# Kernel optimization log

Measured on AMD Instinct MI355X. Metric: run time of the kernel, lower is better.

The kernel has to match this reference:

```python
import jax, jax.numpy as jnp
import numpy as np

N = 50000
IN_DIM = 256
HID = 64
HEADS = 4
OUT_DIM = 64
E = 800000
SLOPE = 0.2


def gat_conv(x, src, dst, W, a_src, a_dst, bias, heads, out_ch):
    """PyG-style GATConv: gather -> edge attention -> segment softmax -> scatter.
    x: [N, in], W: [in, heads*out_ch], a_src/a_dst: [heads, out_ch], bias: [heads*out_ch].
    Returns [N, heads*out_ch] (heads concatenated)."""
    n = x.shape[0]
    h = (x @ W).reshape(n, heads, out_ch)               # [N, H, C]
    s = jnp.einsum('nhc,hc->nh', h, a_src)              # [N, H]
    d = jnp.einsum('nhc,hc->nh', h, a_dst)              # [N, H]
    e = jax.nn.leaky_relu(s[src] + d[dst], SLOPE)       # [E, H]
    emax = jax.ops.segment_max(e, dst, num_segments=n)  # stable softmax per dst
    ex = jnp.exp(e - emax[dst])
    denom = jax.ops.segment_sum(ex, dst, num_segments=n)
    alpha = ex / (denom[dst] + 1e-16)                   # [E, H]
    msg = h[src] * alpha[:, :, None]                    # [E, H, C]
    out = jax.ops.segment_sum(msg, dst, num_segments=n) # [N, H, C]
    return out.reshape(n, heads * out_ch) + bias


def setup_inputs() -> dict:
    key = jax.random.key(0)
    ks = jax.random.split(key, 12)
    x = jax.random.normal(ks[0], (N, IN_DIM), dtype=jnp.float32)
    edge_index = jax.random.randint(ks[1], (2, E), 0, N, dtype=jnp.int64)
    sc = 0.1
    params = {
        'W1': jax.random.normal(ks[2], (IN_DIM, HEADS * HID), dtype=jnp.float32) * sc,
        'a_src1': jax.random.normal(ks[3], (HEADS, HID), dtype=jnp.float32) * sc,
        'a_dst1': jax.random.normal(ks[4], (HEADS, HID), dtype=jnp.float32) * sc,
        'b1': jnp.zeros((HEADS * HID,), dtype=jnp.float32),
        'W2': jax.random.normal(ks[5], (HEADS * HID, HID), dtype=jnp.float32) * sc,
        'a_src2': jax.random.normal(ks[6], (1, HID), dtype=jnp.float32) * sc,
        'a_dst2': jax.random.normal(ks[7], (1, HID), dtype=jnp.float32) * sc,
        'b2': jnp.zeros((HID,), dtype=jnp.float32),
        'Wf1': jax.random.normal(ks[8], (HID, HID), dtype=jnp.float32) * sc,
        'bf1': jnp.zeros((HID,), dtype=jnp.float32),
        'Wf2': jax.random.normal(ks[9], (HID, OUT_DIM), dtype=jnp.float32) * sc,
        'bf2': jnp.zeros((OUT_DIM,), dtype=jnp.float32),
    }
    return {'x': x, 'edge_index': edge_index, **params}


def reference(x, edge_index, W1, a_src1, a_dst1, b1, W2, a_src2, a_dst2, b2,
              Wf1, bf1, Wf2, bf2):
    n = x.shape[0]
    # PyG GATConv adds self-loops by default
    loops = jnp.arange(n, dtype=edge_index.dtype)
    src = jnp.concatenate([edge_index[0], loops])
    dst = jnp.concatenate([edge_index[1], loops])
    h = jax.nn.relu(gat_conv(x, src, dst, W1, a_src1, a_dst1, b1, HEADS, HID))
    h = jax.nn.relu(gat_conv(h, src, dst, W2, a_src2, a_dst2, b2, 1, HID))
    h = jax.nn.relu(h @ Wf1 + bf1)
    return jax.nn.softmax(h @ Wf2 + bf2, axis=1)
```

## Files before the change

kernel.cpp:

```cpp
#include <hip/hip_runtime.h>

#define NNODES 50000
#define NEDGES 800000
#define INDIM  256
#define HIDC   64
#define HEADS  4
static constexpr int ETOT = NEDGES + NNODES;

typedef _Float16 half4 __attribute__((ext_vector_type(4)));
typedef _Float16 half8 __attribute__((ext_vector_type(8)));
typedef short    s16x8 __attribute__((ext_vector_type(8)));
typedef short    s16x4 __attribute__((ext_vector_type(4)));
typedef float    f32x4 __attribute__((ext_vector_type(4)));

__device__ __forceinline__ unsigned short f2bf(float f) {
    unsigned u = __float_as_uint(f);
    u += 0x7fffu + ((u >> 16) & 1u);
    return (unsigned short)(u >> 16);
}
__device__ __forceinline__ float bf2f(unsigned short h) {
    return __uint_as_float(((unsigned)h) << 16);
}

__global__ void detect_k(const unsigned* __restrict__ ei32, int* __restrict__ flag) {
    __shared__ int any32;
    if (threadIdx.x == 0) any32 = 0;
    __syncthreads();
    if (ei32[1 + 2 * threadIdx.x] != 0u) any32 = 1;
    __syncthreads();
    if (threadIdx.x == 0) *flag = !any32;
}

__device__ __forceinline__ int load_idx(const void* ei, int is64, size_t pos) {
    return is64 ? (int)((const long long*)ei)[pos] : ((const int*)ei)[pos];
}

__global__ __launch_bounds__(256)
void hist_k(const void* __restrict__ ei, const int* __restrict__ flag,
            int* __restrict__ count) {
    int e = blockIdx.x * 256 + threadIdx.x;
    if (e >= ETOT) return;
    int is64 = *flag;
    int dst = (e < NEDGES) ? load_idx(ei, is64, (size_t)NEDGES + e) : (e - NEDGES);
    atomicAdd(&count[dst], 1);
}

__global__ __launch_bounds__(1024)
void scan1_k(const int* __restrict__ count, int* __restrict__ rowptr,
             int* __restrict__ bsum, int n) {
    __shared__ int wsum[16];
    const int tid = threadIdx.x;
    const int lane = tid & 63;
    const int w = tid >> 6;
    int i = blockIdx.x * 1024 + tid;
    int v = (i < n) ? count[i] : 0;
    int x = v;
    #pragma unroll
    for (int dd = 1; dd < 64; dd <<= 1) {
        int y = __shfl_up(x, dd);
        if (lane >= dd) x += y;
    }
    if (lane == 63) wsum[w] = x;
    __syncthreads();
    int woff = 0, total = 0;
    #pragma unroll
    for (int j = 0; j < 16; ++j) {
        if (j < w) woff += wsum[j];
        total += wsum[j];
    }
    if (i < n) rowptr[i] = woff + x - v;
    if (tid == 0) bsum[blockIdx.x] = total;
}

__global__ void scan2_k(int* __restrict__ bsum, int* __restrict__ bpre, int nb,
                        int* __restrict__ rowptr, int n) {
    int lane = threadIdx.x;
    int v = (lane < nb) ? bsum[lane] : 0;
    int x = v;
    #pragma unroll
    for (int dd = 1; dd < 64; dd <<= 1) {
        int y = __shfl_up(x, dd);
        if (lane >= dd) x += y;
    }
    if (lane < nb) bpre[lane] = x - v;
    if (lane == 63) rowptr[n] = x;
}

__global__ __launch_bounds__(1024)
void scan3_k(int* __restrict__ rowptr, const int* __restrict__ bpre, int n) {
    int i = blockIdx.x * 1024 + threadIdx.x;
    if (i < n) rowptr[i] += bpre[blockIdx.x];
}

__global__ __launch_bounds__(256)
void scatter_k(const void* __restrict__ ei, const int* __restrict__ flag,
               const int* __restrict__ rowptr, int* __restrict__ fill,
               int* __restrict__ csr_src) {
    int e = blockIdx.x * 256 + threadIdx.x;
    if (e >= ETOT) return;
    int is64 = *flag;
    int src, dst;
    if (e < NEDGES) {
        src = load_idx(ei, is64, (size_t)e);
        dst = load_idx(ei, is64, (size_t)NEDGES + e);
    } else {
        src = e - NEDGES; dst = src;
    }
    int pos = rowptr[dst] + atomicAdd(&fill[dst], 1);
    csr_src[pos] = src;
}

__global__ __launch_bounds__(256)
void convw_k(const float* __restrict__ W, unsigned short* __restrict__ t_hi,
             unsigned short* __restrict__ t_lo, int K, int N) {
    int idx = blockIdx.x * 256 + threadIdx.x;
    if (idx >= K * N) return;
    int k = idx / N, n = idx % N;
    float w = W[idx];
    unsigned short hi = f2bf(w);
    unsigned short lo = f2bf(w - bf2f(hi));
    t_hi[(size_t)n * K + k] = hi;
    t_lo[(size_t)n * K + k] = lo;
}

template<int BN, int SD>
__global__ __launch_bounds__(256)
void gemm_mfma_k(const float* __restrict__ A,
                 const unsigned short* __restrict__ Bt_hi,
                 const unsigned short* __restrict__ Bt_lo,
                 float* __restrict__ C, _Float16* __restrict__ Ch,
                 const float* __restrict__ asrc, const float* __restrict__ adst,
                 float* __restrict__ S, float* __restrict__ D,
                 int M, int N, int K) {
    constexpr int CB = BN / 32;
    constexpr int BI = (BN * 4) / 256;
    __shared__ unsigned short sAh[128][40], sAl[128][40];
    __shared__ unsigned short sBh[BN][40], sBl[BN][40];
    const int tid = threadIdx.x;
    const int bm = blockIdx.y * 128;
    const int bn = blockIdx.x * BN;
    const int w = tid >> 6, lane = tid & 63;
    const int wr = w >> 1, wc = w & 1;
    const int lr = lane & 15, lk = lane >> 4;

    f32x4 acc[4][CB] = {};

    for (int k0 = 0; k0 < K; k0 += 32) {
        float4 av[4];
        #pragma unroll
        for (int i = 0; i < 4; ++i) {
            int idx = tid + 256 * i;
            int row = idx >> 3, c4 = idx & 7;
            int grow = bm + row; if (grow >= M) grow = M - 1;
            av[i] = *(const float4*)(A + (size_t)grow * K + k0 + c4 * 4);
        }
        s16x8 bhv[BI], blv[BI];
        #pragma unroll
        for (int i = 0; i < BI; ++i) {
            int idx = tid + 256 * i;
            int col = idx >> 2, ch = idx & 3;
            bhv[i] = *(const s16x8*)(Bt_hi + (size_t)(bn + col) * K + k0 + ch * 8);
            blv[i] = *(const s16x8*)(Bt_lo + (size_t)(bn + col) * K + k0 + ch * 8);
        }
        __syncthreads();
        #pragma unroll
        for (int i = 0; i < 4; ++i) {
            int idx = tid + 256 * i;
            int row = idx >> 3, c4 = idx & 7;
            float vs[4] = {av[i].x, av[i].y, av[i].z, av[i].w};
            unsigned short h[4], l[4];
            #pragma unroll
            for (int j = 0; j < 4; ++j) {
                h[j] = f2bf(vs[j]);
                l[j] = f2bf(vs[j] - bf2f(h[j]));
            }
            *(s16x4*)&sAh[row][c4 * 4] = (s16x4){(short)h[0], (short)h[1], (short)h[2], (short)h[3]};
            *(s16x4*)&sAl[row][c4 * 4] = (s16x4){(short)l[0], (short)l[1], (short)l[2], (short)l[3]};
        }
        #pragma unroll
        for (int i = 0; i < BI; ++i) {
            int idx = tid + 256 * i;
            int col = idx >> 2, ch = idx & 3;
            *(s16x8*)&sBh[col][ch * 8] = bhv[i];
            *(s16x8*)&sBl[col][ch * 8] = blv[i];
        }
        __syncthreads();
        s16x8 afh[4], afl[4], bfh[CB], bfl[CB];
        #pragma unroll
        for (int rb = 0; rb < 4; ++rb) {
            int row = wr * 64 + rb * 16 + lr;
            afh[rb] = *(const s16x8*)&sAh[row][lk * 8];
            afl[rb] = *(const s16x8*)&sAl[row][lk * 8];
        }
        #pragma unroll
        for (int cb = 0; cb < CB; ++cb) {
            int col = wc * (BN / 2) + cb * 16 + lr;
            bfh[cb] = *(const s16x8*)&sBh[col][lk * 8];
            bfl[cb] = *(const s16x8*)&sBl[col][lk * 8];
        }
        #pragma unroll
        for (int rb = 0; rb < 4; ++rb)
            #pragma unroll
            for (int cb = 0; cb < CB; ++cb) {
                acc[rb][cb] = __builtin_amdgcn_mfma_f32_16x16x32_bf16(afh[rb], bfh[cb], acc[rb][cb], 0, 0, 0);
                acc[rb][cb] = __builtin_amdgcn_mfma_f32_16x16x32_bf16(afh[rb], bfl[cb], acc[rb][cb], 0, 0, 0);
                acc[rb][cb] = __builtin_amdgcn_mfma_f32_16x16x32_bf16(afl[rb], bfh[cb], acc[rb][cb], 0, 0, 0);
            }
    }
    #pragma unroll
    for (int rb = 0; rb < 4; ++rb)
        #pragma unroll
        for (int cb = 0; cb < CB; ++cb)
            #pragma unroll
            for (int r = 0; r < 4; ++r) {
                int row = bm + wr * 64 + rb * 16 + lk * 4 + r;
                int col = bn + wc * (BN / 2) + cb * 16 + lr;
                if (row < M) {
                    float v = acc[rb][cb][r];
                    if constexpr (SD == 0) C[(size_t)row * N + col] = v;
                    if (Ch) Ch[(size_t)row * N + col] = (_Float16)v;
                }
            }
    if constexpr (SD != 0) {
        float af[CB], df[CB];
        #pragma unroll
        for (int cb = 0; cb < CB; ++cb) {
            int colg = bn + wc * (BN / 2) + cb * 16 + lr;
            af[cb] = asrc[colg];
            df[cb] = adst[colg];
        }
        #pragma unroll
        for (int rb = 0; rb < 4; ++rb)
            #pragma unroll
            for (int r = 0; r < 4; ++r) {
                float ps = 0.f, pd = 0.f;
                #pragma unroll
                for (int cb = 0; cb < CB; ++cb) {
                    ps += acc[rb][cb][r] * af[cb];
                    pd += acc[rb][cb][r] * df[cb];
                }
                #pragma unroll
                for (int m = 1; m < 16; m <<= 1) {
                    ps += __shfl_xor(ps, m);
                    pd += __shfl_xor(pd, m);
                }
                int row = bm + wr * 64 + rb * 16 + lk * 4 + r;
                if (lr == 0 && row < M) {
                    if constexpr (SD == 1) {
                        int head = (bn + wc * (BN / 2)) >> 6;
                        S[(size_t)row * (N >> 6) + head] = ps;
                        D[(size_t)row * (N >> 6) + head] = pd;
                    } else {
                        atomicAdd(&S[row], ps);
                        atomicAdd(&D[row], pd);
                    }
                }
            }
    }
}

template<int H>
__global__ __launch_bounds__(256)
void sd_k(const float* __restrict__ hfeat, const float* __restrict__ a_src,
          const float* __restrict__ a_dst, float* __restrict__ s,
          float* __restrict__ d, int n) {
    const int lane = threadIdx.x & 63;
    const int node = blockIdx.x * 4 + (threadIdx.x >> 6);
    if (node >= n) return;
    const float* row = hfeat + (size_t)node * (H * 64);
    #pragma unroll
    for (int h = 0; h < H; ++h) {
        float f = row[h * 64 + lane];
        float vs = f * a_src[h * 64 + lane];
        float vd = f * a_dst[h * 64 + lane];
        #pragma unroll
        for (int m = 32; m; m >>= 1) {
            vs += __shfl_xor(vs, m);
            vd += __shfl_xor(vd, m);
        }
        if (lane == 0) { s[node * H + h] = vs; d[node * H + h] = vd; }
    }
}

__device__ __forceinline__ float leaky(float e) { return (e > 0.f) ? e : 0.2f * e; }

__device__ __forceinline__ float sel4(const float v[4], int idx) {
    float r = v[0];
    r = (idx == 1) ? v[1] : r;
    r = (idx == 2) ? v[2] : r;
    r = (idx == 3) ? v[3] : r;
    return r;
}

__device__ __forceinline__ void osm_upd(float& m, float& sm, float e) {
    float nm = fmaxf(m, e);
    sm = sm * __expf(m - nm) + __expf(e - nm);
    m = nm;
}

template<int H, bool EB>
__global__ __launch_bounds__(256)
void agg_k(const float* __restrict__ hfeat, const _Float16* __restrict__ hhalf,
           const float* __restrict__ s, const float* __restrict__ d,
           const float* __restrict__ bias, const int* __restrict__ rowptr,
           const int* __restrict__ csr_src, float* __restrict__ ebuf,
           float* __restrict__ out, int n) {
    const int lane = threadIdx.x & 63;
    const int node = blockIdx.x * 4 + (threadIdx.x >> 6);
    if (node >= n) return;
    const int beg = rowptr[node];
    const int end = rowptr[node + 1];
    float dh[H], dn[H], inv[H];
    #pragma unroll
    for (int h = 0; h < H; ++h) {
        dh[h] = d[node * H + h];
        dn[h] = 0.f;
    }

    if constexpr (EB) {
        for (int i = beg + lane; i < end; i += 64) {
            int sidx = csr_src[i];
            if constexpr (H == 4) {
                float4 sv = *(const float4*)(s + (size_t)sidx * 4);
                float4 ex;
                ex.x = __expf(leaky(sv.x + dh[0]));
                ex.y = __expf(leaky(sv.y + dh[1]));
                ex.z = __expf(leaky(sv.z + dh[2]));
                ex.w = __expf(leaky(sv.w + dh[3]));
                *(float4*)(ebuf + (size_t)i * 4) = ex;
                dn[0] += ex.x; dn[1] += ex.y; dn[2] += ex.z; dn[3] += ex.w;
            } else {
                float ex = __expf(leaky(s[sidx] + dh[0]));
                ebuf[i] = ex;
                dn[0] += ex;
            }
        }
        #pragma unroll
        for (int h = 0; h < H; ++h) {
            #pragma unroll
            for (int m = 32; m; m >>= 1) dn[h] += __shfl_xor(dn[h], m);
            inv[h] = 1.f / (dn[h] + 1e-16f);
        }

        if constexpr (H == 4) {
            const half8* H8 = (const half8*)hhalf;
            const int sub = lane >> 5;
            const int c8 = lane & 31;
            const int head = c8 >> 3;
            const float invh = sel4(inv, head);
            float acc[8] = {};
            int i = beg;
            for (; i + 7 < end; i += 8) {
                int e0 = i + sub, e1 = i + 2 + sub, e2 = i + 4 + sub, e3 = i + 6 + sub;
                int s0 = csr_src[e0], s1 = csr_src[e1];
                int s2 = csr_src[e2], s3 = csr_src[e3];
                float x0 = ebuf[(size_t)e0 * 4 + head];
                float x1 = ebuf[(size_t)e1 * 4 + head];
                float x2 = ebuf[(size_t)e2 * 4 + head];
                float x3 = ebuf[(size_t)e3 * 4 + head];
                half8 h0 = H8[(size_t)s0 * 32 + c8];
                half8 h1 = H8[(size_t)s1 * 32 + c8];
                half8 h2 = H8[(size_t)s2 * 32 + c8];
                half8 h3 = H8[(size_t)s3 * 32 + c8];
                #pragma unroll
                for (int j = 0; j < 8; ++j)
                    acc[j] += x0 * (float)h0[j] + x1 * (float)h1[j]
                            + x2 * (float)h2[j] + x3 * (float)h3[j];
            }
            for (; i < end; i += 2) {
                int e = i + sub;
                if (e < end) {
                    int s0 = csr_src[e];
                    float x = ebuf[(size_t)e * 4 + head];
                    half8 hh = H8[(size_t)s0 * 32 + c8];
                    #pragma unroll
                    for (int j = 0; j < 8; ++j) acc[j] += x * (float)hh[j];
                }
            }
            #pragma unroll
            for (int j = 0; j < 8; ++j) acc[j] += __shfl_xor(acc[j], 32);
            if (lane < 32) {
                float4 b0 = *(const float4*)(bias + c8 * 8);
                float4 b1 = *(const float4*)(bias + c8 * 8 + 4);
                float4 o0, o1;
                o0.x = fmaxf(acc[0] * invh + b0.x, 0.f);
                o0.y = fmaxf(acc[1] * invh + b0.y, 0.f);
                o0.z = fmaxf(acc[2] * invh + b0.z, 0.f);
                o0.w = fmaxf(acc[3] * invh + b0.w, 0.f);
                o1.x = fmaxf(acc[4] * invh + b1.x, 0.f);
                o1.y = fmaxf(acc[5] * invh + b1.y, 0.f);
                o1.z = fmaxf(acc[6] * invh + b1.z, 0.f);
                o1.w = fmaxf(acc[7] * invh + b1.w, 0.f);
                *(float4*)(out + (size_t)node * 256 + c8 * 8) = o0;
                *(float4*)(out + (size_t)node * 256 + c8 * 8 + 4) = o1;
            }
        } else {
            const half8* H8 = (const half8*)hhalf;
            const int sub = lane >> 3;
            const int c8 = lane & 7;
            float acc[8] = {};
            int i = beg;
            for (; i + 15 < end; i += 16) {
                int e0 = i + sub, e1 = i + 8 + sub;
                int s0 = csr_src[e0], s1 = csr_src[e1];
                float x0 = ebuf[e0], x1 = ebuf[e1];
                half8 h0 = H8[(size_t)s0 * 8 + c8];
                half8 h1 = H8[(size_t)s1 * 8 + c8];
                #pragma unroll
                for (int j = 0; j < 8; ++j)
                    acc[j] += x0 * (float)h0[j] + x1 * (float)h1[j];
            }
            for (; i < end; i += 8) {
                int e = i + sub;
                if (e < end) {
                    int s0 = csr_src[e];
                    float x = ebuf[e];
                    half8 hh = H8[(size_t)s0 * 8 + c8];
                    #pragma unroll
                    for (int j = 0; j < 8; ++j) acc[j] += x * (float)hh[j];
                }
            }
            #pragma unroll
            for (int m = 8; m <= 32; m <<= 1)
                #pragma unroll
                for (int j = 0; j < 8; ++j) acc[j] += __shfl_xor(acc[j], m);
            if (lane < 8) {
                float4 b0 = *(const float4*)(bias + c8 * 8);
                float4 b1 = *(const float4*)(bias + c8 * 8 + 4);
                float4 o0, o1;
                o0.x = fmaxf(acc[0] * inv[0] + b0.x, 0.f);
                o0.y = fmaxf(acc[1] * inv[0] + b0.y, 0.f);
                o0.z = fmaxf(acc[2] * inv[0] + b0.z, 0.f);
                o0.w = fmaxf(acc[3] * inv[0] + b0.w, 0.f);
                o1.x = fmaxf(acc[4] * inv[0] + b1.x, 0.f);
                o1.y = fmaxf(acc[5] * inv[0] + b1.y, 0.f);
                o1.z = fmaxf(acc[6] * inv[0] + b1.z, 0.f);
                o1.w = fmaxf(acc[7] * inv[0] + b1.w, 0.f);
                *(float4*)(out + (size_t)node * 64 + c8 * 8) = o0;
                *(float4*)(out + (size_t)node * 64 + c8 * 8 + 4) = o1;
            }
        }
    } else {
        float mx[H], sm[H];
        #pragma unroll
        for (int h = 0; h < H; ++h) { mx[h] = -3.0e38f; sm[h] = 0.f; }
        for (int i = beg + lane; i < end; i += 64) {
            int sidx = csr_src[i];
            if constexpr (H == 4) {
                float4 sv = *(const float4*)(s + (size_t)sidx * 4);
                osm_upd(mx[0], sm[0], leaky(sv.x + dh[0]));
                osm_upd(mx[1], sm[1], leaky(sv.y + dh[1]));
                osm_upd(mx[2], sm[2], leaky(sv.z + dh[2]));
                osm_upd(mx[3], sm[3], leaky(sv.w + dh[3]));
            } else {
                osm_upd(mx[0], sm[0], leaky(s[sidx] + dh[0]));
            }
        }
        #pragma unroll
        for (int h = 0; h < H; ++h) {
            #pragma unroll
            for (int dd = 32; dd; dd >>= 1) {
                float om = __shfl_xor(mx[h], dd);
                float os = __shfl_xor(sm[h], dd);
                float nm = fmaxf(mx[h], om);
                sm[h] = sm[h] * __expf(mx[h] - nm) + os * __expf(om - nm);
                mx[h] = nm;
            }
            inv[h] = 1.f / (sm[h] + 1e-16f);
        }
        if constexpr (H == 4) {
            const int head = lane >> 4;
            const float invh = sel4(inv, head);
            const float mxh = sel4(mx, head);
            const float dhh = sel4(dh, head);
            const float4* H4 = (const float4*)hfeat;
            float4 acc = {0.f, 0.f, 0.f, 0.f};
            for (int i = beg; i < end; ++i) {
                int s0 = csr_src[i];
                float al0 = __expf(leaky(s[(size_t)s0 * 4 + head] + dhh) - mxh) * invh;
                float4 h0 = H4[(size_t)s0 * 64 + lane];
                acc.x += al0 * h0.x; acc.y += al0 * h0.y;
                acc.z += al0 * h0.z; acc.w += al0 * h0.w;
            }
            float4 bv = ((const float4*)bias)[lane];
            float4 o;
            o.x = fmaxf(acc.x + bv.x, 0.f); o.y = fmaxf(acc.y + bv.y, 0.f);
            o.z = fmaxf(acc.z + bv.z, 0.f); o.w = fmaxf(acc.w + bv.w, 0.f);
            ((float4*)out)[(size_t)node * 64 + lane] = o;
        } else {
            float acc = 0.f;
            for (int i = beg; i < end; ++i) {
                int s0 = csr_src[i];
                float a0 = __expf(leaky(s[s0] + dh[0]) - mx[0]) * inv[0];
                acc += a0 * hfeat[(size_t)s0 * 64 + lane];
            }
            float v = acc + bias[lane];
            out[(size_t)node * 64 + lane] = fmaxf(v, 0.f);
        }
    }
}

__global__ __launch_bounds__(256)
void ffm_k(const float* __restrict__ in,
           const unsigned short* __restrict__ w1h, const unsigned short* __restrict__ w1l,
           const float* __restrict__ bf1,
           const unsigned short* __restrict__ w2h, const unsigned short* __restrict__ w2l,
           const float* __restrict__ bf2, float* __restrict__ out, int M) {
    __shared__ unsigned short sAh[64][80], sAl[64][80];
    __shared__ unsigned short sW1h[64][80], sW1l[64][80];
    __shared__ unsigned short sW2h[64][80], sW2l[64][80];
    const int tid = threadIdx.x;
    const int bm = blockIdx.x * 64;
    const int w = tid >> 6, lane = tid & 63;
    const int lr = lane & 15, lk = lane >> 4;

    for (int c = tid; c < 512; c += 256) {
        int n = c >> 3, k8 = c & 7;
        int dcol = (k8 >> 2) * 40 + (k8 & 3) * 8;
        *(s16x8*)&sW1h[n][dcol] = *(const s16x8*)(w1h + n * 64 + k8 * 8);
        *(s16x8*)&sW1l[n][dcol] = *(const s16x8*)(w1l + n * 64 + k8 * 8);
        *(s16x8*)&sW2h[n][dcol] = *(const s16x8*)(w2h + n * 64 + k8 * 8);
        *(s16x8*)&sW2l[n][dcol] = *(const s16x8*)(w2l + n * 64 + k8 * 8);
    }
    #pragma unroll
    for (int i = 0; i < 4; ++i) {
        int c = tid + 256 * i;
        int row = c >> 4, c4 = c & 15;
        int grow = bm + row; if (grow >= M) grow = M - 1;
        float4 av = *(const float4*)(in + (size_t)grow * 64 + c4 * 4);
        float vs[4] = {av.x, av.y, av.z, av.w};
        unsigned short h[4], l[4];
        #pragma unroll
        for (int j = 0; j < 4; ++j) {
            h[j] = f2bf(vs[j]);
            l[j] = f2bf(vs[j] - bf2f(h[j]));
        }
        int dcol = (c4 >> 3) * 40 + (c4 & 7) * 4;
        *(s16x4*)&sAh[row][dcol] = (s16x4){(short)h[0], (short)h[1], (short)h[2], (short)h[3]};
        *(s16x4*)&sAl[row][dcol] = (s16x4){(short)l[0], (short)l[1], (short)l[2], (short)l[3]};
    }
    __syncthreads();
    f32x4 a1[4] = {};
    #pragma unroll
    for (int ks = 0; ks < 2; ++ks) {
        int koff = ks * 40 + lk * 8;
        s16x8 ah = *(const s16x8*)&sAh[w * 16 + lr][koff];
        s16x8 al = *(const s16x8*)&sAl[w * 16 + lr][koff];
        #pragma unroll
        for (int cb = 0; cb < 4; ++cb) {
            s16x8 bh = *(const s16x8*)&sW1h[cb * 16 + lr][koff];
            s16x8 bl = *(const s16x8*)&sW1l[cb * 16 + lr][koff];
            a1[cb] = __builtin_amdgcn_mfma_f32_16x16x32_bf16(ah, bh, a1[cb], 0, 0, 0);
            a1[cb] = __builtin_amdgcn_mfma_f32_16x16x32_bf16(ah, bl, a1[cb], 0, 0, 0);
            a1[cb] = __builtin_amdgcn_mfma_f32_16x16x32_bf16(al, bh, a1[cb], 0, 0, 0);
        }
    }
    __syncthreads();
    #pragma unroll
    for (int cb = 0; cb < 4; ++cb) {
        int col = cb * 16 + lr;
        float b = bf1[col];
        int dcol = (col >> 5) * 40 + (col & 31);
        #pragma unroll
        for (int r = 0; r < 4; ++r) {
            int row = w * 16 + lk * 4 + r;
            float y = fmaxf(a1[cb][r] + b, 0.f);
            unsigned short hh = f2bf(y);
            sAh[row][dcol] = hh;
            sAl[row][dcol] = f2bf(y - bf2f(hh));
        }
    }
    __syncthreads();
    f32x4 a2[4] = {};
    #pragma unroll
    for (int ks = 0; ks < 2; ++ks) {
        int koff = ks * 40 + lk * 8;
        s16x8 ah = *(const s16x8*)&sAh[w * 16 + lr][koff];
        s16x8 al = *(const s16x8*)&sAl[w * 16 + lr][koff];
        #pragma unroll
        for (int cb = 0; cb < 4; ++cb) {
            s16x8 bh = *(const s16x8*)&sW2h[cb * 16 + lr][koff];
            s16x8 bl = *(const s16x8*)&sW2l[cb * 16 + lr][koff];
            a2[cb] = __builtin_amdgcn_mfma_f32_16x16x32_bf16(ah, bh, a2[cb], 0, 0, 0);
            a2[cb] = __builtin_amdgcn_mfma_f32_16x16x32_bf16(ah, bl, a2[cb], 0, 0, 0);
            a2[cb] = __builtin_amdgcn_mfma_f32_16x16x32_bf16(al, bh, a2[cb], 0, 0, 0);
        }
    }
    float zb[4];
    #pragma unroll
    for (int cb = 0; cb < 4; ++cb) zb[cb] = bf2[cb * 16 + lr];
    #pragma unroll
    for (int r = 0; r < 4; ++r) {
        int row = bm + w * 16 + lk * 4 + r;
        float z0 = a2[0][r] + zb[0], z1 = a2[1][r] + zb[1];
        float z2 = a2[2][r] + zb[2], z3 = a2[3][r] + zb[3];
        float m = fmaxf(fmaxf(z0, z1), fmaxf(z2, z3));
        #pragma unroll
        for (int dd = 1; dd < 16; dd <<= 1) m = fmaxf(m, __shfl_xor(m, dd));
        float e0 = __expf(z0 - m), e1 = __expf(z1 - m);
        float e2 = __expf(z2 - m), e3 = __expf(z3 - m);
        float sum = e0 + e1 + e2 + e3;
        #pragma unroll
        for (int dd = 1; dd < 16; dd <<= 1) sum += __shfl_xor(sum, dd);
        float is = 1.f / sum;
        if (row < M) {
            out[(size_t)row * 64 + 0 + lr]  = e0 * is;
            out[(size_t)row * 64 + 16 + lr] = e1 * is;
            out[(size_t)row * 64 + 32 + lr] = e2 * is;
            out[(size_t)row * 64 + 48 + lr] = e3 * is;
        }
    }
}

__global__ __launch_bounds__(256)
void ff_k(const float* __restrict__ in, const float* __restrict__ Wf1,
          const float* __restrict__ bf1, const float* __restrict__ Wf2,
          const float* __restrict__ bf2, float* __restrict__ out, int n) {
    __shared__ float w1[64 * 64];
    __shared__ float w2[64 * 64];
    __shared__ float xrow[4][64];
    __shared__ float yrow[4][64];
    const int tid = threadIdx.x;
    for (int i = tid; i < 64 * 64; i += 256) { w1[i] = Wf1[i]; w2[i] = Wf2[i]; }
    __syncthreads();
    const int wv = tid >> 6;
    const int lane = tid & 63;
    const float B1 = bf1[lane], B2 = bf2[lane];
    const int nblk = (n + 3) / 4;
    for (int nb = blockIdx.x; nb < nblk; nb += gridDim.x) {
        int node = nb * 4 + wv;
        int nd = node < n ? node : (n - 1);
        float x = in[(size_t)nd * 64 + lane];
        xrow[wv][lane] = x;
        float y = B1;
        #pragma unroll 8
        for (int k = 0; k < 64; ++k) y += xrow[wv][k] * w1[k * 64 + lane];
        y = fmaxf(y, 0.f);
        yrow[wv][lane] = y;
        float z = B2;
        #pragma unroll 8
        for (int k = 0; k < 64; ++k) z += yrow[wv][k] * w2[k * 64 + lane];
        float m = z;
        #pragma unroll
        for (int dd = 32; dd; dd >>= 1) m = fmaxf(m, __shfl_xor(m, dd));
        float ex = __expf(z - m);
        float sum = ex;
        #pragma unroll
        for (int dd = 32; dd; dd >>= 1) sum += __shfl_xor(sum, dd);
        if (node < n) out[(size_t)node * 64 + lane] = ex / sum;
    }
}

extern "C" void kernel_launch(void* const* d_in, const int* in_sizes, int n_in,
                              void* d_out, int out_size, void* d_ws, size_t ws_size,
                              hipStream_t stream) {
    const float* x      = (const float*)d_in[0];
    const void*  ei     = d_in[1];
    const float* W1     = (const float*)d_in[2];
    const float* a_src1 = (const float*)d_in[3];
    const float* a_dst1 = (const float*)d_in[4];
    const float* b1     = (const float*)d_in[5];
    const float* W2     = (const float*)d_in[6];
    const float* a_src2 = (const float*)d_in[7];
    const float* a_dst2 = (const float*)d_in[8];
    const float* b2     = (const float*)d_in[9];
    const float* Wf1    = (const float*)d_in[10];
    const float* bf1    = (const float*)d_in[11];
    const float* Wf2    = (const float*)d_in[12];
    const float* bf2    = (const float*)d_in[13];
    float* outp = (float*)d_out;

    char* ws = (char*)d_ws;
    size_t off = 0;
    auto take = [&](size_t bytes) -> char* {
        char* p = ws + off;
        off += (bytes + 255) & ~(size_t)255;
        return p;
    };
    int*   flag   = (int*)take(4);
    int*   count  = (int*)take((size_t)NNODES * 4);
    int*   fill   = (int*)take((size_t)NNODES * 4);
    int*   rowptr = (int*)take((size_t)(NNODES + 1) * 4);
    int*   bsum   = (int*)take(64 * 4);
    int*   bpre   = (int*)take(64 * 4);
    int*   csr    = (int*)take((size_t)ETOT * 4);
    unsigned short* w1t_hi = (unsigned short*)take((size_t)256 * 256 * 2);
    unsigned short* w1t_lo = (unsigned short*)take((size_t)256 * 256 * 2);
    unsigned short* w2t_hi = (unsigned short*)take((size_t)64 * 256 * 2);
    unsigned short* w2t_lo = (unsigned short*)take((size_t)64 * 256 * 2);
    unsigned short* wf1t_hi = (unsigned short*)take((size_t)64 * 64 * 2);
    unsigned short* wf1t_lo = (unsigned short*)take((size_t)64 * 64 * 2);
    unsigned short* wf2t_hi = (unsigned short*)take((size_t)64 * 64 * 2);
    unsigned short* wf2t_lo = (unsigned short*)take((size_t)64 * 64 * 2);
    float* h1     = (float*)take((size_t)NNODES * 256 * 4);
    float* agg1   = (float*)take((size_t)NNODES * 256 * 4);
    float* s1     = (float*)take((size_t)NNODES * HEADS * 4);
    float* d1     = (float*)take((size_t)NNODES * HEADS * 4);
    float* ebuf   = (float*)take((size_t)ETOT * HEADS * 4);
    _Float16* h1h = (_Float16*)take((size_t)NNODES * 256 * 2);
    const bool eb_ok = (off <= ws_size);
    float*    h2   = h1;
    float*    s2   = s1;
    float*    d2   = d1;
    float*    agg2 = agg1;
    _Float16* h2h  = h1h;

    detect_k<<<1, 128, 0, stream>>>((const unsigned*)ei, flag);
    hipMemsetAsync(count, 0, (size_t)NNODES * 4, stream);
    hipMemsetAsync(fill, 0, (size_t)NNODES * 4, stream);
    const int eblocks = (ETOT + 255) / 256;
    hist_k<<<eblocks, 256, 0, stream>>>(ei, flag, count);
    const int sblocks = (NNODES + 1023) / 1024;
    scan1_k<<<sblocks, 1024, 0, stream>>>(count, rowptr, bsum, NNODES);
    scan2_k<<<1, 64, 0, stream>>>(bsum, bpre, sblocks, rowptr, NNODES);
    scan3_k<<<sblocks, 1024, 0, stream>>>(rowptr, bpre, NNODES);
    scatter_k<<<eblocks, 256, 0, stream>>>(ei, flag, rowptr, fill, csr);

    convw_k<<<(256 * 256) / 256, 256, 0, stream>>>(W1, w1t_hi, w1t_lo, 256, 256);
    convw_k<<<(256 * 64) / 256, 256, 0, stream>>>(W2, w2t_hi, w2t_lo, 256, 64);
    convw_k<<<(64 * 64) / 256, 256, 0, stream>>>(Wf1, wf1t_hi, wf1t_lo, 64, 64);
    convw_k<<<(64 * 64) / 256, 256, 0, stream>>>(Wf2, wf2t_hi, wf2t_lo, 64, 64);

    const int nodeblocks = NNODES / 4;
    const int mblocks = (NNODES + 127) / 128;
    const dim3 gg1(2, mblocks);
    const dim3 gg2(1, mblocks);

    if (eb_ok) {
        gemm_mfma_k<128, 1><<<gg1, 256, 0, stream>>>(x, w1t_hi, w1t_lo,
            nullptr, h1h, a_src1, a_dst1, s1, d1, NNODES, 256, 256);
        agg_k<HEADS, true><<<nodeblocks, 256, 0, stream>>>(h1, h1h, s1, d1, b1,
            rowptr, csr, ebuf, agg1, NNODES);

        hipMemsetAsync(s2, 0, (size_t)NNODES * 4, stream);
        hipMemsetAsync(d2, 0, (size_t)NNODES * 4, stream);
        gemm_mfma_k<64, 2><<<gg2, 256, 0, stream>>>(agg1, w2t_hi, w2t_lo,
            nullptr, h2h, a_src2, a_dst2, s2, d2, NNODES, 64, 256);
        agg_k<1, true><<<nodeblocks, 256, 0, stream>>>(h2, h2h, s2, d2, b2,
            rowptr, csr, ebuf, agg2, NNODES);

        ffm_k<<<(NNODES + 63) / 64, 256, 0, stream>>>(agg2, wf1t_hi, wf1t_lo,
            bf1, wf2t_hi, wf2t_lo, bf2, outp, NNODES);
    } else {
        gemm_mfma_k<128, 0><<<gg1, 256, 0, stream>>>(x, w1t_hi, w1t_lo,
            h1, nullptr, nullptr, nullptr, nullptr, nullptr, NNODES, 256, 256);
        sd_k<HEADS><<<nodeblocks, 256, 0, stream>>>(h1, a_src1, a_dst1, s1, d1, NNODES);
        agg_k<HEADS, false><<<nodeblocks, 256, 0, stream>>>(h1, h1h, s1, d1, b1,
            rowptr, csr, ebuf, agg1, NNODES);
        gemm_mfma_k<64, 0><<<gg2, 256, 0, stream>>>(agg1, w2t_hi, w2t_lo,
            h2, nullptr, nullptr, nullptr, nullptr, nullptr, NNODES, 64, 256);
        sd_k<1><<<nodeblocks, 256, 0, stream>>>(h2, a_src2, a_dst2, s2, d2, NNODES);
        agg_k<1, false><<<nodeblocks, 256, 0, stream>>>(h2, h2h, s2, d2, b2,
            rowptr, csr, ebuf, agg2, NNODES);
        ff_k<<<1024, 256, 0, stream>>>(agg2, Wf1, bf1, Wf2, bf2, outp, NNODES);
    }
}
```

Before: 291.7 us.

## Drop edge buffer, stage edge weights in LDS, merge setup launches

The aggregation kernel no longer writes per-edge exp values to a global edge buffer and rereads them. It now processes each node's edges in chunks of 64, keeping source indices and exp weights in per-wave shared memory, and normalises by the denominator only at the end. Several small launches are also merged: the index-width detection is inlined into the edge kernels, the four weight conversions become one kernel, and paired memsets are combined. The fallback path and the fp32 feature buffers are removed. Relying on s_waitcnt rather than a barrier for the wave-private LDS is a subtle correctness assumption.

```diff
diff --git a/kernel.cpp b/kernel.cpp
--- a/kernel.cpp
+++ b/kernel.cpp
@@ -7,7 +7,6 @@
 #define HEADS  4
 static constexpr int ETOT = NEDGES + NNODES;
 
-typedef _Float16 half4 __attribute__((ext_vector_type(4)));
 typedef _Float16 half8 __attribute__((ext_vector_type(8)));
 typedef short    s16x8 __attribute__((ext_vector_type(8)));
 typedef short    s16x4 __attribute__((ext_vector_type(4)));
@@ -22,13 +21,11 @@
     return __uint_as_float(((unsigned)h) << 16);
 }
 
-__global__ void detect_k(const unsigned* __restrict__ ei32, int* __restrict__ flag) {
-    __shared__ int any32;
-    if (threadIdx.x == 0) any32 = 0;
-    __syncthreads();
-    if (ei32[1 + 2 * threadIdx.x] != 0u) any32 = 1;
-    __syncthreads();
-    if (threadIdx.x == 0) *flag = !any32;
+__device__ __forceinline__ int is_int64(const unsigned* __restrict__ ei32) {
+    int r = 1;
+    #pragma unroll
+    for (int i = 1; i < 64; i += 2) r &= (ei32[i] == 0u);
+    return r;
 }
 
 __device__ __forceinline__ int load_idx(const void* ei, int is64, size_t pos) {
@@ -36,11 +33,10 @@
 }
 
 __global__ __launch_bounds__(256)
-void hist_k(const void* __restrict__ ei, const int* __restrict__ flag,
-            int* __restrict__ count) {
+void hist_k(const void* __restrict__ ei, int* __restrict__ count) {
     int e = blockIdx.x * 256 + threadIdx.x;
     if (e >= ETOT) return;
-    int is64 = *flag;
+    int is64 = is_int64((const unsigned*)ei);
     int dst = (e < NEDGES) ? load_idx(ei, is64, (size_t)NEDGES + e) : (e - NEDGES);
     atomicAdd(&count[dst], 1);
 }
@@ -93,12 +89,11 @@
 }
 
 __global__ __launch_bounds__(256)
-void scatter_k(const void* __restrict__ ei, const int* __restrict__ flag,
-               const int* __restrict__ rowptr, int* __restrict__ fill,
-               int* __restrict__ csr_src) {
+void scatter_k(const void* __restrict__ ei, const int* __restrict__ rowptr,
+               int* __restrict__ fill, int* __restrict__ csr_src) {
     int e = blockIdx.x * 256 + threadIdx.x;
     if (e >= ETOT) return;
-    int is64 = *flag;
+    int is64 = is_int64((const unsigned*)ei);
     int src, dst;
     if (e < NEDGES) {
         src = load_idx(ei, is64, (size_t)e);
@@ -111,16 +106,25 @@
 }
 
 __global__ __launch_bounds__(256)
-void convw_k(const float* __restrict__ W, unsigned short* __restrict__ t_hi,
-             unsigned short* __restrict__ t_lo, int K, int N) {
+void convall_k(const float* __restrict__ W1, const float* __restrict__ W2,
+               const float* __restrict__ Wf1, const float* __restrict__ Wf2,
+               unsigned short* __restrict__ w1h, unsigned short* __restrict__ w1l,
+               unsigned short* __restrict__ w2h, unsigned short* __restrict__ w2l,
+               unsigned short* __restrict__ f1h, unsigned short* __restrict__ f1l,
+               unsigned short* __restrict__ f2h, unsigned short* __restrict__ f2l) {
     int idx = blockIdx.x * 256 + threadIdx.x;
-    if (idx >= K * N) return;
+    const float* W; unsigned short *th, *tl; int K, N;
+    if (idx < 65536)       { W = W1;  th = w1h; tl = w1l; K = 256; N = 256; }
+    else if (idx < 81920)  { idx -= 65536; W = W2;  th = w2h; tl = w2l; K = 256; N = 64; }
+    else if (idx < 86016)  { idx -= 81920; W = Wf1; th = f1h; tl = f1l; K = 64;  N = 64; }
+    else if (idx < 90112)  { idx -= 86016; W = Wf2; th = f2h; tl = f2l; K = 64;  N = 64; }
+    else return;
     int k = idx / N, n = idx % N;
-    float w = W[idx];
+    float w = W[(size_t)k * N + n];
     unsigned short hi = f2bf(w);
     unsigned short lo = f2bf(w - bf2f(hi));
-    t_hi[(size_t)n * K + k] = hi;
-    t_lo[(size_t)n * K + k] = lo;
+    th[(size_t)n * K + k] = hi;
+    tl[(size_t)n * K + k] = lo;
 }
 
 template<int BN, int SD>
@@ -128,7 +132,7 @@
 void gemm_mfma_k(const float* __restrict__ A,
                  const unsigned short* __restrict__ Bt_hi,
                  const unsigned short* __restrict__ Bt_lo,
-                 float* __restrict__ C, _Float16* __restrict__ Ch,
+                 _Float16* __restrict__ Ch,
                  const float* __restrict__ asrc, const float* __restrict__ adst,
                  float* __restrict__ S, float* __restrict__ D,
                  int M, int N, int K) {
@@ -215,13 +219,9 @@
             for (int r = 0; r < 4; ++r) {
                 int row = bm + wr * 64 + rb * 16 + lk * 4 + r;
                 int col = bn + wc * (BN / 2) + cb * 16 + lr;
-                if (row < M) {
-                    float v = acc[rb][cb][r];
-                    if constexpr (SD == 0) C[(size_t)row * N + col] = v;
-                    if (Ch) Ch[(size_t)row * N + col] = (_Float16)v;
-                }
-            }
-    if constexpr (SD != 0) {
+                if (row < M) Ch[(size_t)row * N + col] = (_Float16)acc[rb][cb][r];
+            }
+    {
         float af[CB], df[CB];
         #pragma unroll
         for (int cb = 0; cb < CB; ++cb) {
@@ -259,29 +259,6 @@
     }
 }
 
-template<int H>
-__global__ __launch_bounds__(256)
-void sd_k(const float* __restrict__ hfeat, const float* __restrict__ a_src,
-          const float* __restrict__ a_dst, float* __restrict__ s,
-          float* __restrict__ d, int n) {
-    const int lane = threadIdx.x & 63;
-    const int node = blockIdx.x * 4 + (threadIdx.x >> 6);
-    if (node >= n) return;
-    const float* row = hfeat + (size_t)node * (H * 64);
-    #pragma unroll
-    for (int h = 0; h < H; ++h) {
-        float f = row[h * 64 + lane];
-        float vs = f * a_src[h * 64 + lane];
-        float vd = f * a_dst[h * 64 + lane];
-        #pragma unroll
-        for (int m = 32; m; m >>= 1) {
-            vs += __shfl_xor(vs, m);
-            vd += __shfl_xor(vd, m);
-        }
-        if (lane == 0) { s[node * H + h] = vs; d[node * H + h] = vd; }
-    }
-}
-
 __device__ __forceinline__ float leaky(float e) { return (e > 0.f) ? e : 0.2f * e; }
 
 __device__ __forceinline__ float sel4(const float v[4], int idx) {
@@ -292,210 +269,154 @@
     return r;
 }
 
-__device__ __forceinline__ void osm_upd(float& m, float& sm, float e) {
-    float nm = fmaxf(m, e);
-    sm = sm * __expf(m - nm) + __expf(e - nm);
-    m = nm;
-}
-
-template<int H, bool EB>
+template<int H>
 __global__ __launch_bounds__(256)
-void agg_k(const float* __restrict__ hfeat, const _Float16* __restrict__ hhalf,
+void agg_k(const _Float16* __restrict__ hhalf,
            const float* __restrict__ s, const float* __restrict__ d,
            const float* __restrict__ bias, const int* __restrict__ rowptr,
-           const int* __restrict__ csr_src, float* __restrict__ ebuf,
-           float* __restrict__ out, int n) {
+           const int* __restrict__ csr_src, float* __restrict__ out, int n) {
+    __shared__ float exs[4][H][64];
+    __shared__ int   srcs[4][64];
     const int lane = threadIdx.x & 63;
-    const int node = blockIdx.x * 4 + (threadIdx.x >> 6);
+    const int wv   = threadIdx.x >> 6;
+    const int node = blockIdx.x * 4 + wv;
     if (node >= n) return;
-    const int beg = rowptr[node];
-    const int end = rowptr[node + 1];
-    float dh[H], dn[H], inv[H];
-    #pragma unroll
-    for (int h = 0; h < H; ++h) {
-        dh[h] = d[node * H + h];
-        dn[h] = 0.f;
-    }
-
-    if constexpr (EB) {
-        for (int i = beg + lane; i < end; i += 64) {
-            int sidx = csr_src[i];
-            if constexpr (H == 4) {
+    const int beg = rowptr[node], end = rowptr[node + 1];
+    float dh[H], dn[H];
+    #pragma unroll
+    for (int h = 0; h < H; ++h) { dh[h] = d[node * H + h]; dn[h] = 0.f; }
+    const half8* H8 = (const half8*)hhalf;
+
+    if constexpr (H == 4) {
+        const int sub = lane >> 5, c8 = lane & 31, head = c8 >> 3;
+        float acc[8] = {};
+        for (int c0 = beg; c0 < end; c0 += 64) {
+            const int cend = (c0 + 64 < end) ? c0 + 64 : end;
+            int e = c0 + lane;
+            if (e < end) {
+                int sidx = csr_src[e];
                 float4 sv = *(const float4*)(s + (size_t)sidx * 4);
-                float4 ex;
-                ex.x = __expf(leaky(sv.x + dh[0]));
-                ex.y = __expf(leaky(sv.y + dh[1]));
-                ex.z = __expf(leaky(sv.z + dh[2]));
-                ex.w = __expf(leaky(sv.w + dh[3]));
-                *(float4*)(ebuf + (size_t)i * 4) = ex;
-                dn[0] += ex.x; dn[1] += ex.y; dn[2] += ex.z; dn[3] += ex.w;
-            } else {
-                float ex = __expf(leaky(s[sidx] + dh[0]));
-                ebuf[i] = ex;
-                dn[0] += ex;
-            }
-        }
-        #pragma unroll
-        for (int h = 0; h < H; ++h) {
-            #pragma unroll
-            for (int m = 32; m; m >>= 1) dn[h] += __shfl_xor(dn[h], m);
-            inv[h] = 1.f / (dn[h] + 1e-16f);
-        }
-
-        if constexpr (H == 4) {
-            const half8* H8 = (const half8*)hhalf;
-            const int sub = lane >> 5;
-            const int c8 = lane & 31;
-            const int head = c8 >> 3;
-            const float invh = sel4(inv, head);
-            float acc[8] = {};
-            int i = beg;
-            for (; i + 7 < end; i += 8) {
-                int e0 = i + sub, e1 = i + 2 + sub, e2 = i + 4 + sub, e3 = i + 6 + sub;
-                int s0 = csr_src[e0], s1 = csr_src[e1];
-                int s2 = csr_src[e2], s3 = csr_src[e3];
-                float x0 = ebuf[(size_t)e0 * 4 + head];
-                float x1 = ebuf[(size_t)e1 * 4 + head];
-                float x2 = ebuf[(size_t)e2 * 4 + head];
-                float x3 = ebuf[(size_t)e3 * 4 + head];
+                float e0 = __expf(leaky(sv.x + dh[0]));
+                float e1 = __expf(leaky(sv.y + dh[1]));
+                float e2 = __expf(leaky(sv.z + dh[2]));
+                float e3 = __expf(leaky(sv.w + dh[3]));
+                srcs[wv][lane] = sidx;
+                exs[wv][0][lane] = e0; exs[wv][1][lane] = e1;
+                exs[wv][2][lane] = e2; exs[wv][3][lane] = e3;
+                dn[0] += e0; dn[1] += e1; dn[2] += e2; dn[3] += e3;
+            }
+            asm volatile("s_waitcnt lgkmcnt(0)" ::: "memory");
+            int i = c0;
+            for (; i + 7 < cend; i += 8) {
+                int j = i - c0 + sub;
+                int s0 = srcs[wv][j],     s1 = srcs[wv][j + 2];
+                int s2 = srcs[wv][j + 4], s3 = srcs[wv][j + 6];
+                float x0 = exs[wv][head][j],     x1 = exs[wv][head][j + 2];
+                float x2 = exs[wv][head][j + 4], x3 = exs[wv][head][j + 6];
                 half8 h0 = H8[(size_t)s0 * 32 + c8];
                 half8 h1 = H8[(size_t)s1 * 32 + c8];
                 half8 h2 = H8[(size_t)s2 * 32 + c8];
                 half8 h3 = H8[(size_t)s3 * 32 + c8];
                 #pragma unroll
-                for (int j = 0; j < 8; ++j)
-                    acc[j] += x0 * (float)h0[j] + x1 * (float)h1[j]
-                            + x2 * (float)h2[j] + x3 * (float)h3[j];
-            }
-            for (; i < end; i += 2) {
-                int e = i + sub;
-                if (e < end) {
-                    int s0 = csr_src[e];
-                    float x = ebuf[(size_t)e * 4 + head];
+                for (int q = 0; q < 8; ++q)
+                    acc[q] += x0 * (float)h0[q] + x1 * (float)h1[q]
+                            + x2 * (float)h2[q] + x3 * (float)h3[q];
+            }
+            for (; i < cend; i += 2) {
+                int e2i = i + sub;
+                if (e2i < cend) {
+                    int j = e2i - c0;
+                    int s0 = srcs[wv][j];
+                    float x = exs[wv][head][j];
                     half8 hh = H8[(size_t)s0 * 32 + c8];
                     #pragma unroll
-                    for (int j = 0; j < 8; ++j) acc[j] += x * (float)hh[j];
+                    for (int q = 0; q < 8; ++q) acc[q] += x * (float)hh[q];
                 }
             }
+        }
+        float inv_[4];
+        #pragma unroll
+        for (int h = 0; h < 4; ++h) {
             #pragma unroll
-            for (int j = 0; j < 8; ++j) acc[j] += __shfl_xor(acc[j], 32);
-            if (lane < 32) {
-                float4 b0 = *(const float4*)(bias + c8 * 8);
-                float4 b1 = *(const float4*)(bias + c8 * 8 + 4);
-                float4 o0, o1;
-                o0.x = fmaxf(acc[0] * invh + b0.x, 0.f);
-                o0.y = fmaxf(acc[1] * invh + b0.y, 0.f);
-                o0.z = fmaxf(acc[2] * invh + b0.z, 0.f);
-                o0.w = fmaxf(acc[3] * invh + b0.w, 0.f);
-                o1.x = fmaxf(acc[4] * invh + b1.x, 0.f);
-                o1.y = fmaxf(acc[5] * invh + b1.y, 0.f);
-                o1.z = fmaxf(acc[6] * invh + b1.z, 0.f);
-                o1.w = fmaxf(acc[7] * invh + b1.w, 0.f);
-                *(float4*)(out + (size_t)node * 256 + c8 * 8) = o0;
-                *(float4*)(out + (size_t)node * 256 + c8 * 8 + 4) = o1;
-            }
-        } else {
-            const half8* H8 = (const half8*)hhalf;
-            const int sub = lane >> 3;
-            const int c8 = lane & 7;
-            float acc[8] = {};
-            int i = beg;
-            for (; i + 15 < end; i += 16) {
-                int e0 = i + sub, e1 = i + 8 + sub;
-                int s0 = csr_src[e0], s1 = csr_src[e1];
-                float x0 = ebuf[e0], x1 = ebuf[e1];
+            for (int m = 32; m; m >>= 1) dn[h] += __shfl_xor(dn[h], m);
+            inv_[h] = 1.f / (dn[h] + 1e-16f);
+        }
+        const float invh = sel4(inv_, head);
+        #pragma unroll
+        for (int q = 0; q < 8; ++q) acc[q] += __shfl_xor(acc[q], 32);
+        if (lane < 32) {
+            float4 b0 = *(const float4*)(bias + c8 * 8);
+            float4 b1 = *(const float4*)(bias + c8 * 8 + 4);
+            float4 o0, o1;
+            o0.x = fmaxf(acc[0] * invh + b0.x, 0.f);
+            o0.y = fmaxf(acc[1] * invh + b0.y, 0.f);
+            o0.z = fmaxf(acc[2] * invh + b0.z, 0.f);
+            o0.w = fmaxf(acc[3] * invh + b0.w, 0.f);
+            o1.x = fmaxf(acc[4] * invh + b1.x, 0.f);
+            o1.y = fmaxf(acc[5] * invh + b1.y, 0.f);
+            o1.z = fmaxf(acc[6] * invh + b1.z, 0.f);
+            o1.w = fmaxf(acc[7] * invh + b1.w, 0.f);
+            *(float4*)(out + (size_t)node * 256 + c8 * 8) = o0;
+            *(float4*)(out + (size_t)node * 256 + c8 * 8 + 4) = o1;
+        }
+    } else {
+        const int sub = lane >> 3, c8 = lane & 7;
+        float acc[8] = {};
+        for (int c0 = beg; c0 < end; c0 += 64) {
+            const int cend = (c0 + 64 < end) ? c0 + 64 : end;
+            int e = c0 + lane;
+            if (e < end) {
+                int sidx = csr_src[e];
+                float ex = __expf(leaky(s[sidx] + dh[0]));
+                srcs[wv][lane] = sidx;
+                exs[wv][0][lane] = ex;
+                dn[0] += ex;
+            }
+            asm volatile("s_waitcnt lgkmcnt(0)" ::: "memory");
+            int i = c0;
+            for (; i + 15 < cend; i += 16) {
+                int j = i - c0 + sub;
+                int s0 = srcs[wv][j], s1 = srcs[wv][j + 8];
+                float x0 = exs[wv][0][j], x1 = exs[wv][0][j + 8];
                 half8 h0 = H8[(size_t)s0 * 8 + c8];
                 half8 h1 = H8[(size_t)s1 * 8 + c8];
                 #pragma unroll
-                for (int j = 0; j < 8; ++j)
-                    acc[j] += x0 * (float)h0[j] + x1 * (float)h1[j];
-            }
-            for (; i < end; i += 8) {
-                int e = i + sub;
-                if (e < end) {
-                    int s0 = csr_src[e];
-                    float x = ebuf[e];
+                for (int q = 0; q < 8; ++q)
+                    acc[q] += x0 * (float)h0[q] + x1 * (float)h1[q];
+            }
+            for (; i < cend; i += 8) {
+                int e2i = i + sub;
+                if (e2i < cend) {
+                    int j = e2i - c0;
+                    int s0 = srcs[wv][j];
+                    float x = exs[wv][0][j];
                     half8 hh = H8[(size_t)s0 * 8 + c8];
                     #pragma unroll
-                    for (int j = 0; j < 8; ++j) acc[j] += x * (float)hh[j];
+                    for (int q = 0; q < 8; ++q) acc[q] += x * (float)hh[q];
                 }
             }
+        }
+        #pragma unroll
+        for (int m = 32; m; m >>= 1) dn[0] += __shfl_xor(dn[0], m);
+        const float inv0 = 1.f / (dn[0] + 1e-16f);
+        #pragma unroll
+        for (int m = 8; m <= 32; m <<= 1)
             #pragma unroll
-            for (int m = 8; m <= 32; m <<= 1)
-                #pragma unroll
-                for (int j = 0; j < 8; ++j) acc[j] += __shfl_xor(acc[j], m);
-            if (lane < 8) {
-                float4 b0 = *(const float4*)(bias + c8 * 8);
-                float4 b1 = *(const float4*)(bias + c8 * 8 + 4);
-                float4 o0, o1;
-                o0.x = fmaxf(acc[0] * inv[0] + b0.x, 0.f);
-                o0.y = fmaxf(acc[1] * inv[0] + b0.y, 0.f);
-                o0.z = fmaxf(acc[2] * inv[0] + b0.z, 0.f);
-                o0.w = fmaxf(acc[3] * inv[0] + b0.w, 0.f);
-                o1.x = fmaxf(acc[4] * inv[0] + b1.x, 0.f);
-                o1.y = fmaxf(acc[5] * inv[0] + b1.y, 0.f);
-                o1.z = fmaxf(acc[6] * inv[0] + b1.z, 0.f);
-                o1.w = fmaxf(acc[7] * inv[0] + b1.w, 0.f);
-                *(float4*)(out + (size_t)node * 64 + c8 * 8) = o0;
-                *(float4*)(out + (size_t)node * 64 + c8 * 8 + 4) = o1;
-            }
-        }
-    } else {
-        float mx[H], sm[H];
-        #pragma unroll
-        for (int h = 0; h < H; ++h) { mx[h] = -3.0e38f; sm[h] = 0.f; }
-        for (int i = beg + lane; i < end; i += 64) {
-            int sidx = csr_src[i];
-            if constexpr (H == 4) {
-                float4 sv = *(const float4*)(s + (size_t)sidx * 4);
-                osm_upd(mx[0], sm[0], leaky(sv.x + dh[0]));
-                osm_upd(mx[1], sm[1], leaky(sv.y + dh[1]));
-                osm_upd(mx[2], sm[2], leaky(sv.z + dh[2]));
-                osm_upd(mx[3], sm[3], leaky(sv.w + dh[3]));
-            } else {
-                osm_upd(mx[0], sm[0], leaky(s[sidx] + dh[0]));
-            }
-        }
-        #pragma unroll
-        for (int h = 0; h < H; ++h) {
-            #pragma unroll
-            for (int dd = 32; dd; dd >>= 1) {
-                float om = __shfl_xor(mx[h], dd);
-                float os = __shfl_xor(sm[h], dd);
-                float nm = fmaxf(mx[h], om);
-                sm[h] = sm[h] * __expf(mx[h] - nm) + os * __expf(om - nm);
-                mx[h] = nm;
-            }
-            inv[h] = 1.f / (sm[h] + 1e-16f);
-        }
-        if constexpr (H == 4) {
-            const int head = lane >> 4;
-            const float invh = sel4(inv, head);
-            const float mxh = sel4(mx, head);
-            const float dhh = sel4(dh, head);
-            const float4* H4 = (const float4*)hfeat;
-            float4 acc = {0.f, 0.f, 0.f, 0.f};
-            for (int i = beg; i < end; ++i) {
-                int s0 = csr_src[i];
-                float al0 = __expf(leaky(s[(size_t)s0 * 4 + head] + dhh) - mxh) * invh;
-                float4 h0 = H4[(size_t)s0 * 64 + lane];
-                acc.x += al0 * h0.x; acc.y += al0 * h0.y;
-                acc.z += al0 * h0.z; acc.w += al0 * h0.w;
-            }
-            float4 bv = ((const float4*)bias)[lane];
-            float4 o;
-            o.x = fmaxf(acc.x + bv.x, 0.f); o.y = fmaxf(acc.y + bv.y, 0.f);
-            o.z = fmaxf(acc.z + bv.z, 0.f); o.w = fmaxf(acc.w + bv.w, 0.f);
-            ((float4*)out)[(size_t)node * 64 + lane] = o;
-        } else {
-            float acc = 0.f;
-            for (int i = beg; i < end; ++i) {
-                int s0 = csr_src[i];
-                float a0 = __expf(leaky(s[s0] + dh[0]) - mx[0]) * inv[0];
-                acc += a0 * hfeat[(size_t)s0 * 64 + lane];
-            }
-            float v = acc + bias[lane];
-            out[(size_t)node * 64 + lane] = fmaxf(v, 0.f);
+            for (int q = 0; q < 8; ++q) acc[q] += __shfl_xor(acc[q], m);
+        if (lane < 8) {
+            float4 b0 = *(const float4*)(bias + c8 * 8);
+            float4 b1 = *(const float4*)(bias + c8 * 8 + 4);
+            float4 o0, o1;
+            o0.x = fmaxf(acc[0] * inv0 + b0.x, 0.f);
+            o0.y = fmaxf(acc[1] * inv0 + b0.y, 0.f);
+            o0.z = fmaxf(acc[2] * inv0 + b0.z, 0.f);
+            o0.w = fmaxf(acc[3] * inv0 + b0.w, 0.f);
+            o1.x = fmaxf(acc[4] * inv0 + b1.x, 0.f);
+            o1.y = fmaxf(acc[5] * inv0 + b1.y, 0.f);
+            o1.z = fmaxf(acc[6] * inv0 + b1.z, 0.f);
+            o1.w = fmaxf(acc[7] * inv0 + b1.w, 0.f);
+            *(float4*)(out + (size_t)node * 64 + c8 * 8) = o0;
+            *(float4*)(out + (size_t)node * 64 + c8 * 8 + 4) = o1;
         }
     }
 }
@@ -609,45 +530,6 @@
             out[(size_t)row * 64 + 32 + lr] = e2 * is;
             out[(size_t)row * 64 + 48 + lr] = e3 * is;
         }
-    }
-}
-
-__global__ __launch_bounds__(256)
-void ff_k(const float* __restrict__ in, const float* __restrict__ Wf1,
-          const float* __restrict__ bf1, const float* __restrict__ Wf2,
-          const float* __restrict__ bf2, float* __restrict__ out, int n) {
-    __shared__ float w1[64 * 64];
-    __shared__ float w2[64 * 64];
-    __shared__ float xrow[4][64];
-    __shared__ float yrow[4][64];
-    const int tid = threadIdx.x;
-    for (int i = tid; i < 64 * 64; i += 256) { w1[i] = Wf1[i]; w2[i] = Wf2[i]; }
-    __syncthreads();
-    const int wv = tid >> 6;
-    const int lane = tid & 63;
-    const float B1 = bf1[lane], B2 = bf2[lane];
-    const int nblk = (n + 3) / 4;
-    for (int nb = blockIdx.x; nb < nblk; nb += gridDim.x) {
-        int node = nb * 4 + wv;
-        int nd = node < n ? node : (n - 1);
-        float x = in[(size_t)nd * 64 + lane];
-        xrow[wv][lane] = x;
-        float y = B1;
-        #pragma unroll 8
-        for (int k = 0; k < 64; ++k) y += xrow[wv][k] * w1[k * 64 + lane];
-        y = fmaxf(y, 0.f);
-        yrow[wv][lane] = y;
-        float z = B2;
-        #pragma unroll 8
-        for (int k = 0; k < 64; ++k) z += yrow[wv][k] * w2[k * 64 + lane];
-        float m = z;
-        #pragma unroll
-        for (int dd = 32; dd; dd >>= 1) m = fmaxf(m, __shfl_xor(m, dd));
-        float ex = __expf(z - m);
-        float sum = ex;
-        #pragma unroll
-        for (int dd = 32; dd; dd >>= 1) sum += __shfl_xor(sum, dd);
-        if (node < n) out[(size_t)node * 64 + lane] = ex / sum;
     }
 }
 
@@ -677,7 +559,6 @@
         off += (bytes + 255) & ~(size_t)255;
         return p;
     };
-    int*   flag   = (int*)take(4);
     int*   count  = (int*)take((size_t)NNODES * 4);
     int*   fill   = (int*)take((size_t)NNODES * 4);
     int*   rowptr = (int*)take((size_t)(NNODES + 1) * 4);
@@ -692,66 +573,44 @@
     unsigned short* wf1t_lo = (unsigned short*)take((size_t)64 * 64 * 2);
     unsigned short* wf2t_hi = (unsigned short*)take((size_t)64 * 64 * 2);
     unsigned short* wf2t_lo = (unsigned short*)take((size_t)64 * 64 * 2);
-    float* h1     = (float*)take((size_t)NNODES * 256 * 4);
     float* agg1   = (float*)take((size_t)NNODES * 256 * 4);
     float* s1     = (float*)take((size_t)NNODES * HEADS * 4);
     float* d1     = (float*)take((size_t)NNODES * HEADS * 4);
-    float* ebuf   = (float*)take((size_t)ETOT * HEADS * 4);
     _Float16* h1h = (_Float16*)take((size_t)NNODES * 256 * 2);
-    const bool eb_ok = (off <= ws_size);
-    float*    h2   = h1;
     float*    s2   = s1;
     float*    d2   = d1;
     float*    agg2 = agg1;
     _Float16* h2h  = h1h;
 
-    detect_k<<<1, 128, 0, stream>>>((const unsigned*)ei, flag);
-    hipMemsetAsync(count, 0, (size_t)NNODES * 4, stream);
-    hipMemsetAsync(fill, 0, (size_t)NNODES * 4, stream);
+    hipMemsetAsync(count, 0, (size_t)((char*)fill - (char*)count) + (size_t)NNODES * 4, stream);
     const int eblocks = (ETOT + 255) / 256;
-    hist_k<<<eblocks, 256, 0, stream>>>(ei, flag, count);
+    hist_k<<<eblocks, 256, 0, stream>>>(ei, count);
     const int sblocks = (NNODES + 1023) / 1024;
     scan1_k<<<sblocks, 1024, 0, stream>>>(count, rowptr, bsum, NNODES);
     scan2_k<<<1, 64, 0, stream>>>(bsum, bpre, sblocks, rowptr, NNODES);
     scan3_k<<<sblocks, 1024, 0, stream>>>(rowptr, bpre, NNODES);
-    scatter_k<<<eblocks, 256, 0, stream>>>(ei, flag, rowptr, fill, csr);
-
-    convw_k<<<(256 * 256) / 256, 256, 0, stream>>>(W1, w1t_hi, w1t_lo, 256, 256);
-    convw_k<<<(256 * 64) / 256, 256, 0, stream>>>(W2, w2t_hi, w2t_lo, 256, 64);
-    convw_k<<<(64 * 64) / 256, 256, 0, stream>>>(Wf1, wf1t_hi, wf1t_lo, 64, 64);
-    convw_k<<<(64 * 64) / 256, 256, 0, stream>>>(Wf2, wf2t_hi, wf2t_lo, 64, 64);
+    scatter_k<<<eblocks, 256, 0, stream>>>(ei, rowptr, fill, csr);
+
+    convall_k<<<(90112 + 255) / 256, 256, 0, stream>>>(
+        W1, W2, Wf1, Wf2, w1t_hi, w1t_lo, w2t_hi, w2t_lo,
+        wf1t_hi, wf1t_lo, wf2t_hi, wf2t_lo);
 
     const int nodeblocks = NNODES / 4;
     const int mblocks = (NNODES + 127) / 128;
     const dim3 gg1(2, mblocks);
     const dim3 gg2(1, mblocks);
 
-    if (eb_ok) {
-        gemm_mfma_k<128, 1><<<gg1, 256, 0, stream>>>(x, w1t_hi, w1t_lo,
-            nullptr, h1h, a_src1, a_dst1, s1, d1, NNODES, 256, 256);
-        agg_k<HEADS, true><<<nodeblocks, 256, 0, stream>>>(h1, h1h, s1, d1, b1,
-            rowptr, csr, ebuf, agg1, NNODES);
-
-        hipMemsetAsync(s2, 0, (size_t)NNODES * 4, stream);
-        hipMemsetAsync(d2, 0, (size_t)NNODES * 4, stream);
-        gemm_mfma_k<64, 2><<<gg2, 256, 0, stream>>>(agg1, w2t_hi, w2t_lo,
-            nullptr, h2h, a_src2, a_dst2, s2, d2, NNODES, 64, 256);
-        agg_k<1, true><<<nodeblocks, 256, 0, stream>>>(h2, h2h, s2, d2, b2,
-            rowptr, csr, ebuf, agg2, NNODES);
-
-        ffm_k<<<(NNODES + 63) / 64, 256, 0, stream>>>(agg2, wf1t_hi, wf1t_lo,
-            bf1, wf2t_hi, wf2t_lo, bf2, outp, NNODES);
-    } else {
-        gemm_mfma_k<128, 0><<<gg1, 256, 0, stream>>>(x, w1t_hi, w1t_lo,
-            h1, nullptr, nullptr, nullptr, nullptr, nullptr, NNODES, 256, 256);
-        sd_k<HEADS><<<nodeblocks, 256, 0, stream>>>(h1, a_src1, a_dst1, s1, d1, NNODES);
-        agg_k<HEADS, false><<<nodeblocks, 256, 0, stream>>>(h1, h1h, s1, d1, b1,
-            rowptr, csr, ebuf, agg1, NNODES);
-        gemm_mfma_k<64, 0><<<gg2, 256, 0, stream>>>(agg1, w2t_hi, w2t_lo,
-            h2, nullptr, nullptr, nullptr, nullptr, nullptr, NNODES, 64, 256);
-        sd_k<1><<<nodeblocks, 256, 0, stream>>>(h2, a_src2, a_dst2, s2, d2, NNODES);
-        agg_k<1, false><<<nodeblocks, 256, 0, stream>>>(h2, h2h, s2, d2, b2,
-            rowptr, csr, ebuf, agg2, NNODES);
-        ff_k<<<1024, 256, 0, stream>>>(agg2, Wf1, bf1, Wf2, bf2, outp, NNODES);
-    }
-}
+    gemm_mfma_k<128, 1><<<gg1, 256, 0, stream>>>(x, w1t_hi, w1t_lo,
+        h1h, a_src1, a_dst1, s1, d1, NNODES, 256, 256);
+    agg_k<HEADS><<<nodeblocks, 256, 0, stream>>>(h1h, s1, d1, b1,
+        rowptr, csr, agg1, NNODES);
+
+    hipMemsetAsync(s2, 0, (size_t)((char*)d1 - (char*)s1) + (size_t)NNODES * 4, stream);
+    gemm_mfma_k<64, 2><<<gg2, 256, 0, stream>>>(agg1, w2t_hi, w2t_lo,
+        h2h, a_src2, a_dst2, s2, d2, NNODES, 64, 256);
+    agg_k<1><<<nodeblocks, 256, 0, stream>>>(h2h, s2, d2, b2,
+        rowptr, csr, agg2, NNODES);
+
+    ffm_k<<<(NNODES + 63) / 64, 256, 0, stream>>>(agg2, wf1t_hi, wf1t_lo,
+        bf1, wf2t_hi, wf2t_lo, bf2, outp, NNODES);
+}
```

New measurement: 280.3 us. 1.04x faster.
